# Kernel optimization log

Hardware: AMD Instinct MI355X
Metric: run time of the kernel (lower is better)

## Reference

```python
import jax, jax.numpy as jnp
import numpy as np

def setup_inputs() -> dict:
    key = jax.random.key(0)
    k1, k2, k3 = jax.random.split(key, 3)
    N, C, H, W = 16, 128, 128, 128
    out_chn = 128
    x = jax.random.normal(k1, (N, C, H, W), dtype=jnp.float32)
    # 1x1 conv = per-pixel linear: weight (out_chn, in_chn), bias (out_chn,)
    fan_in = C  # kernel_size=1 -> fan_in = in_chn
    bound = 1.0 / np.sqrt(fan_in)
    conv_w = jax.random.uniform(k2, (out_chn, C), dtype=jnp.float32, minval=-bound, maxval=bound)
    conv_b = jax.random.uniform(k3, (out_chn,), dtype=jnp.float32, minval=-bound, maxval=bound)
    return {"x": x, "conv_w": conv_w, "conv_b": conv_b}

def reference(x, conv_w, conv_b):
    N, C, H, W = x.shape
    x_hw = x.reshape(N, C, H * W)                     # (N, C, HW)
    logits = jnp.einsum('ncl,ndl->ncd', x_hw, x_hw)    # (N, C, C), unscaled
    weights = jax.nn.softmax(logits, axis=-1)
    attn = jnp.einsum('ncd,ndl->ncl', weights, x_hw)   # (N, C, HW)
    attn = attn.reshape(N, C, H, W)
    # 1x1 conv: contract over channel dim
    out = jnp.einsum('nchw,oc->nohw', attn, conv_w) + conv_b[None, :, None, None]
    return out
```

## Files before the change

kernel.cpp:

```cpp
#include <hip/hip_runtime.h>
#include <stdint.h>

#define NB    16
#define CD    128
#define HW    16384
#define KSPLIT 32

typedef float  f32x4  __attribute__((ext_vector_type(4)));
typedef short  bf16x8 __attribute__((ext_vector_type(8)));

__device__ __forceinline__ unsigned f2bf(float f) {
    unsigned u = __float_as_uint(f);
    u += 0x7FFFu + ((u >> 16) & 1u);
    return u >> 16;
}
__device__ __forceinline__ unsigned pk2bf(float a, float b) {
    return f2bf(a) | (f2bf(b) << 16);
}

__global__ __launch_bounds__(256, 2) void gram_kernel(const float* __restrict__ x,
                                                      float* __restrict__ P) {
    const int n  = blockIdx.x;
    const int kc = blockIdx.y;
    const int t    = threadIdx.x;
    const int wv   = t >> 6;
    const int lane = t & 63;
    const int q    = lane >> 4;
    const int r16  = lane & 15;

    __shared__ __align__(16) unsigned short Xl[2 * CD * 128];

    f32x4 acc[4][4];
#pragma unroll
    for (int i = 0; i < 4; ++i)
#pragma unroll
        for (int j = 0; j < 4; ++j) acc[i][j] = (f32x4)0.0f;

    const int rt0 = 4 * (wv >> 1);
    const int ct0 = 4 * (wv & 1);

    const float* xb = x + (size_t)n * CD * HW;

    const int cS  = t >> 5;
    const int lS  = (t & 31) * 4;
    const int wsw = lS ^ (8 * cS);
    const int rx  = 8 * (r16 & 7);

    float4 stg[16];
#pragma unroll
    for (int i = 0; i < 16; ++i)
        stg[i] = *(const float4*)(xb + (size_t)(i * 8 + cS) * HW + kc * 512 + lS);
#pragma unroll
    for (int i = 0; i < 16; ++i) {
        uint2 pk;
        pk.x = pk2bf(stg[i].x, stg[i].y);
        pk.y = pk2bf(stg[i].z, stg[i].w);
        *(uint2*)(&Xl[(i * 8 + cS) * 128 + wsw]) = pk;
    }

    for (int sub = 0; sub < 4; ++sub) {
        if (sub < 3) {
            const int kb = kc * 512 + (sub + 1) * 128;
#pragma unroll
            for (int i = 0; i < 16; ++i)
                stg[i] = *(const float4*)(xb + (size_t)(i * 8 + cS) * HW + kb + lS);
        }
        __syncthreads();

        const unsigned short* Xc = &Xl[(size_t)(sub & 1) * CD * 128];
#pragma unroll
        for (int ks = 0; ks < 4; ++ks) {
            const int ko = (ks * 32 + q * 8) ^ rx;
            bf16x8 af[4], bfr[4];
#pragma unroll
            for (int i = 0; i < 4; ++i) {
                union { bf16x8 v; uint4 u; } ua;
                ua.u = *(const uint4*)&Xc[(16 * (rt0 + i) + r16) * 128 + ko];
                af[i] = ua.v;
                union { bf16x8 v; uint4 u; } ub;
                ub.u = *(const uint4*)&Xc[(16 * (ct0 + i) + r16) * 128 + ko];
                bfr[i] = ub.v;
            }
#pragma unroll
            for (int i = 0; i < 4; ++i)
#pragma unroll
                for (int j = 0; j < 4; ++j)
                    acc[i][j] = __builtin_amdgcn_mfma_f32_16x16x32_bf16(
                        af[i], bfr[j], acc[i][j], 0, 0, 0);
        }

        if (sub < 3) {
            unsigned short* Xn = &Xl[(size_t)((sub + 1) & 1) * CD * 128];
#pragma unroll
            for (int i = 0; i < 16; ++i) {
                uint2 pk;
                pk.x = pk2bf(stg[i].x, stg[i].y);
                pk.y = pk2bf(stg[i].z, stg[i].w);
                *(uint2*)(&Xn[(i * 8 + cS) * 128 + wsw]) = pk;
            }
        }
    }

    float* Pn = P + ((size_t)kc * NB + n) * CD * CD;
#pragma unroll
    for (int i = 0; i < 4; ++i)
#pragma unroll
        for (int j = 0; j < 4; ++j)
#pragma unroll
            for (int rr = 0; rr < 4; ++rr) {
                int row = 16 * (rt0 + i) + q * 4 + rr;
                int col = 16 * (ct0 + j) + r16;
                Pn[row * CD + col] = acc[i][j][rr];
            }
}

__global__ __launch_bounds__(256) void reduce_kernel(const float* __restrict__ P,
                                                     float* __restrict__ E) {
    const int R    = blockIdx.x * 4 + (threadIdx.x >> 6);
    const int lane = threadIdx.x & 63;
    const int n    = R >> 7;
    const int row  = R & 127;

    const float* p = P + (size_t)n * CD * CD + (size_t)row * CD + 2 * lane;
    float s0 = 0.0f, s1 = 0.0f;
#pragma unroll
    for (int kc = 0; kc < KSPLIT; ++kc) {
        const float2 v = *(const float2*)(p + (size_t)kc * NB * CD * CD);
        s0 += v.x; s1 += v.y;
    }
    float m = fmaxf(s0, s1);
#pragma unroll
    for (int off = 32; off > 0; off >>= 1) m = fmaxf(m, __shfl_xor(m, off));
    const float e0 = __expf(s0 - m);
    const float e1 = __expf(s1 - m);
    float e = e0 + e1;
#pragma unroll
    for (int off = 32; off > 0; off >>= 1) e += __shfl_xor(e, off);
    const float inv = 1.0f / e;
    float2 st; st.x = e0 * inv; st.y = e1 * inv;
    *(float2*)(E + (size_t)n * CD * CD + (size_t)row * CD + 2 * lane) = st;
}

__global__ __launch_bounds__(256) void mmat_kernel(const float* __restrict__ E,
                                                   const float* __restrict__ cw,
                                                   unsigned short* __restrict__ Mbf) {
    const int n  = blockIdx.x;
    const int bo = blockIdx.y;
    const int t  = threadIdx.x;
    const int o  = bo * 8 + (t >> 5);
    const int d0 = (t & 31) * 4;

    const float* En  = E + (size_t)n * CD * CD;
    const float* cwo = cw + (size_t)o * CD;

    float a0 = 0, a1 = 0, a2 = 0, a3 = 0;
#pragma unroll 8
    for (int c = 0; c < CD; ++c) {
        const float cv = cwo[c];
        float4 w = *(const float4*)&En[c * CD + d0];
        a0 += cv * w.x; a1 += cv * w.y; a2 += cv * w.z; a3 += cv * w.w;
    }
    uint2 pk;
    pk.x = pk2bf(a0, a1);
    pk.y = pk2bf(a2, a3);
    *(uint2*)&Mbf[((size_t)n * CD + o) * CD + d0] = pk;
}

__global__ __launch_bounds__(256) void out_kernel(const float* __restrict__ x,
                                                  const unsigned short* __restrict__ Mbf,
                                                  const float* __restrict__ bias,
                                                  float* __restrict__ out) {
    const int lb = blockIdx.x;
    const int n  = blockIdx.y;
    const int l0 = lb * 128;
    const int t    = threadIdx.x;
    const int wv   = t >> 6;
    const int lane = t & 63;
    const int q    = lane >> 4;
    const int r16  = lane & 15;

    __shared__ __align__(16) unsigned short Xt[128 * 128];
    __shared__ float bl[CD];

    const int lt0 = 4 * (wv >> 1);
    const int ot0 = 4 * (wv & 1);

    if (t < CD) bl[t] = bias[t];

    const float* xb = x + (size_t)n * CD * HW + l0;
    const int lt = t & 31;
    const int dg = t >> 5;
#pragma unroll
    for (int i = 0; i < 4; ++i) {
        const int d0 = i * 32 + dg * 4;
        const float* bp = xb + (size_t)d0 * HW + 4 * lt;
        float4 v0 = *(const float4*)(bp);
        float4 v1 = *(const float4*)(bp + HW);
        float4 v2 = *(const float4*)(bp + 2 * HW);
        float4 v3 = *(const float4*)(bp + 3 * HW);
        float r0[4] = {v0.x, v0.y, v0.z, v0.w};
        float r1[4] = {v1.x, v1.y, v1.z, v1.w};
        float r2[4] = {v2.x, v2.y, v2.z, v2.w};
        float r3[4] = {v3.x, v3.y, v3.z, v3.w};
        const int dph = d0 ^ (8 * (lt & 7));
#pragma unroll
        for (int j = 0; j < 4; ++j) {
            uint2 pk;
            pk.x = pk2bf(r0[j], r1[j]);
            pk.y = pk2bf(r2[j], r3[j]);
            *(uint2*)&Xt[(4 * lt + j) * 128 + dph] = pk;
        }
    }
    __syncthreads();

    f32x4 acc[4][4];
#pragma unroll
    for (int i = 0; i < 4; ++i)
#pragma unroll
        for (int j = 0; j < 4; ++j) acc[i][j] = (f32x4)0.0f;

    const unsigned short* Mn = Mbf + (size_t)n * CD * CD;
#pragma unroll
    for (int ks = 0; ks < 4; ++ks) {
        const int k0 = ks * 32 + q * 8;
        bf16x8 bfr[4];
#pragma unroll
        for (int j = 0; j < 4; ++j) {
            const int o = 16 * (ot0 + j) + r16;
            union { bf16x8 v; uint4 u; } ub;
            ub.u = *(const uint4*)&Mn[o * CD + k0];
            bfr[j] = ub.v;
        }
        bf16x8 af[4];
#pragma unroll
        for (int i = 0; i < 4; ++i) {
            const int l = 16 * (lt0 + i) + r16;
            const int doff = k0 ^ (8 * ((l >> 2) & 7));
            union { bf16x8 v; uint4 u; } ua;
            ua.u = *(const uint4*)&Xt[l * 128 + doff];
            af[i] = ua.v;
        }
#pragma unroll
        for (int i = 0; i < 4; ++i)
#pragma unroll
            for (int j = 0; j < 4; ++j)
                acc[i][j] = __builtin_amdgcn_mfma_f32_16x16x32_bf16(
                    af[i], bfr[j], acc[i][j], 0, 0, 0);
    }

    float* ob = out + (size_t)n * CD * HW + l0;
#pragma unroll
    for (int i = 0; i < 4; ++i)
#pragma unroll
        for (int j = 0; j < 4; ++j) {
            const int o = 16 * (ot0 + j) + r16;
            const int l = 16 * (lt0 + i) + q * 4;
            const float b = bl[o];
            float4 st;
            st.x = acc[i][j][0] + b;
            st.y = acc[i][j][1] + b;
            st.z = acc[i][j][2] + b;
            st.w = acc[i][j][3] + b;
            *(float4*)(ob + (size_t)o * HW + l) = st;
        }
}

extern "C" void kernel_launch(void* const* d_in, const int* in_sizes, int n_in,
                              void* d_out, int out_size, void* d_ws, size_t ws_size,
                              hipStream_t stream) {
    const float* x  = (const float*)d_in[0];
    const float* cw = (const float*)d_in[1];
    const float* cb = (const float*)d_in[2];
    float* out = (float*)d_out;

    char* ws = (char*)d_ws;
    float*          P   = (float*)(ws);
    float*          E   = (float*)(ws + (32u << 20));
    unsigned short* Mbf = (unsigned short*)(ws + (33u << 20));

    gram_kernel   <<<dim3(NB, KSPLIT), 256, 0, stream>>>(x, P);
    reduce_kernel <<<dim3(512),        256, 0, stream>>>(P, E);
    mmat_kernel   <<<dim3(NB, 16),     256, 0, stream>>>(E, cw, Mbf);
    out_kernel    <<<dim3(128, NB),    256, 0, stream>>>(x, Mbf, cb, out);
}
```

Baseline: 300.8 us.

## Fuse reduce, mmat and output kernels into one persistent ticketed tail kernel

Replaces three separate launches (softmax reduce, mixing-matrix build, output GEMM) with a single kernel whose blocks take atomic tickets and synchronize through global counters, spin-waiting on flags between stages. Flags are reset by the first gram block. This removes two kernel launch boundaries and lets output blocks start staging x as soon as dependencies resolve, at the cost of spin-wait overhead and a reliance on ticket ordering for forward progress.

New measurement: 665.1 us. 2.21x slower.

```diff
diff --git a/kernel.cpp b/kernel.cpp
--- a/kernel.cpp
+++ b/kernel.cpp
@@ -19,7 +19,8 @@
 }
 
 __global__ __launch_bounds__(256, 2) void gram_kernel(const float* __restrict__ x,
-                                                      float* __restrict__ P) {
+                                                      float* __restrict__ P,
+                                                      unsigned* __restrict__ flags) {
     const int n  = blockIdx.x;
     const int kc = blockIdx.y;
     const int t    = threadIdx.x;
@@ -28,13 +29,9 @@
     const int q    = lane >> 4;
     const int r16  = lane & 15;
 
+    if (n == 0 && kc == 0 && t < 3) flags[t * 16] = 0u;
+
     __shared__ __align__(16) unsigned short Xl[2 * CD * 128];
-
-    f32x4 acc[4][4];
-#pragma unroll
-    for (int i = 0; i < 4; ++i)
-#pragma unroll
-        for (int j = 0; j < 4; ++j) acc[i][j] = (f32x4)0.0f;
 
     const int rt0 = 4 * (wv >> 1);
     const int ct0 = 4 * (wv & 1);
@@ -45,6 +42,12 @@
     const int lS  = (t & 31) * 4;
     const int wsw = lS ^ (8 * cS);
     const int rx  = 8 * (r16 & 7);
+
+    f32x4 acc[4][4];
+#pragma unroll
+    for (int i = 0; i < 4; ++i)
+#pragma unroll
+        for (int j = 0; j < 4; ++j) acc[i][j] = (f32x4)0.0f;
 
     float4 stg[16];
 #pragma unroll
@@ -114,155 +117,176 @@
             }
 }
 
-__global__ __launch_bounds__(256) void reduce_kernel(const float* __restrict__ P,
-                                                     float* __restrict__ E) {
-    const int R    = blockIdx.x * 4 + (threadIdx.x >> 6);
-    const int lane = threadIdx.x & 63;
-    const int n    = R >> 7;
-    const int row  = R & 127;
-
-    const float* p = P + (size_t)n * CD * CD + (size_t)row * CD + 2 * lane;
-    float s0 = 0.0f, s1 = 0.0f;
-#pragma unroll
-    for (int kc = 0; kc < KSPLIT; ++kc) {
-        const float2 v = *(const float2*)(p + (size_t)kc * NB * CD * CD);
-        s0 += v.x; s1 += v.y;
-    }
-    float m = fmaxf(s0, s1);
-#pragma unroll
-    for (int off = 32; off > 0; off >>= 1) m = fmaxf(m, __shfl_xor(m, off));
-    const float e0 = __expf(s0 - m);
-    const float e1 = __expf(s1 - m);
-    float e = e0 + e1;
-#pragma unroll
-    for (int off = 32; off > 0; off >>= 1) e += __shfl_xor(e, off);
-    const float inv = 1.0f / e;
-    float2 st; st.x = e0 * inv; st.y = e1 * inv;
-    *(float2*)(E + (size_t)n * CD * CD + (size_t)row * CD + 2 * lane) = st;
-}
-
-__global__ __launch_bounds__(256) void mmat_kernel(const float* __restrict__ E,
-                                                   const float* __restrict__ cw,
-                                                   unsigned short* __restrict__ Mbf) {
-    const int n  = blockIdx.x;
-    const int bo = blockIdx.y;
-    const int t  = threadIdx.x;
-    const int o  = bo * 8 + (t >> 5);
-    const int d0 = (t & 31) * 4;
-
-    const float* En  = E + (size_t)n * CD * CD;
-    const float* cwo = cw + (size_t)o * CD;
-
-    float a0 = 0, a1 = 0, a2 = 0, a3 = 0;
-#pragma unroll 8
-    for (int c = 0; c < CD; ++c) {
-        const float cv = cwo[c];
-        float4 w = *(const float4*)&En[c * CD + d0];
-        a0 += cv * w.x; a1 += cv * w.y; a2 += cv * w.z; a3 += cv * w.w;
-    }
-    uint2 pk;
-    pk.x = pk2bf(a0, a1);
-    pk.y = pk2bf(a2, a3);
-    *(uint2*)&Mbf[((size_t)n * CD + o) * CD + d0] = pk;
-}
-
-__global__ __launch_bounds__(256) void out_kernel(const float* __restrict__ x,
-                                                  const unsigned short* __restrict__ Mbf,
-                                                  const float* __restrict__ bias,
-                                                  float* __restrict__ out) {
-    const int lb = blockIdx.x;
-    const int n  = blockIdx.y;
-    const int l0 = lb * 128;
-    const int t    = threadIdx.x;
-    const int wv   = t >> 6;
-    const int lane = t & 63;
-    const int q    = lane >> 4;
-    const int r16  = lane & 15;
-
+__global__ __launch_bounds__(256, 4) void tail_kernel(
+    const float* __restrict__ P, const float* __restrict__ x,
+    const float* __restrict__ cw, const float* __restrict__ cb,
+    float* __restrict__ E, unsigned short* __restrict__ Mbf,
+    float* __restrict__ out, unsigned* __restrict__ flags)
+{
+    const int t = threadIdx.x;
+    __shared__ unsigned s_tk;
     __shared__ __align__(16) unsigned short Xt[128 * 128];
     __shared__ float bl[CD];
 
-    const int lt0 = 4 * (wv >> 1);
-    const int ot0 = 4 * (wv & 1);
-
-    if (t < CD) bl[t] = bias[t];
-
-    const float* xb = x + (size_t)n * CD * HW + l0;
-    const int lt = t & 31;
-    const int dg = t >> 5;
-#pragma unroll
-    for (int i = 0; i < 4; ++i) {
-        const int d0 = i * 32 + dg * 4;
-        const float* bp = xb + (size_t)d0 * HW + 4 * lt;
-        float4 v0 = *(const float4*)(bp);
-        float4 v1 = *(const float4*)(bp + HW);
-        float4 v2 = *(const float4*)(bp + 2 * HW);
-        float4 v3 = *(const float4*)(bp + 3 * HW);
-        float r0[4] = {v0.x, v0.y, v0.z, v0.w};
-        float r1[4] = {v1.x, v1.y, v1.z, v1.w};
-        float r2[4] = {v2.x, v2.y, v2.z, v2.w};
-        float r3[4] = {v3.x, v3.y, v3.z, v3.w};
-        const int dph = d0 ^ (8 * (lt & 7));
-#pragma unroll
-        for (int j = 0; j < 4; ++j) {
-            uint2 pk;
-            pk.x = pk2bf(r0[j], r1[j]);
-            pk.y = pk2bf(r2[j], r3[j]);
-            *(uint2*)&Xt[(4 * lt + j) * 128 + dph] = pk;
-        }
-    }
+    if (t == 0) s_tk = atomicAdd(&flags[0], 1u);
     __syncthreads();
-
-    f32x4 acc[4][4];
-#pragma unroll
-    for (int i = 0; i < 4; ++i)
-#pragma unroll
-        for (int j = 0; j < 4; ++j) acc[i][j] = (f32x4)0.0f;
-
-    const unsigned short* Mn = Mbf + (size_t)n * CD * CD;
-#pragma unroll
-    for (int ks = 0; ks < 4; ++ks) {
-        const int k0 = ks * 32 + q * 8;
-        bf16x8 bfr[4];
-#pragma unroll
-        for (int j = 0; j < 4; ++j) {
-            const int o = 16 * (ot0 + j) + r16;
-            union { bf16x8 v; uint4 u; } ub;
-            ub.u = *(const uint4*)&Mn[o * CD + k0];
-            bfr[j] = ub.v;
-        }
-        bf16x8 af[4];
+    const unsigned tk = s_tk;
+
+    if (tk < 512u) {
+        const int R    = (int)tk * 4 + (t >> 6);
+        const int lane = t & 63;
+        const int n    = R >> 7;
+        const int row  = R & 127;
+        const float* p = P + (size_t)n * CD * CD + (size_t)row * CD + 2 * lane;
+        float s0 = 0.0f, s1 = 0.0f;
+#pragma unroll
+        for (int kc = 0; kc < KSPLIT; ++kc) {
+            const float2 v = *(const float2*)(p + (size_t)kc * NB * CD * CD);
+            s0 += v.x; s1 += v.y;
+        }
+        float m = fmaxf(s0, s1);
+#pragma unroll
+        for (int off = 32; off > 0; off >>= 1) m = fmaxf(m, __shfl_xor(m, off));
+        const float e0 = __expf(s0 - m);
+        const float e1 = __expf(s1 - m);
+        float e = e0 + e1;
+#pragma unroll
+        for (int off = 32; off > 0; off >>= 1) e += __shfl_xor(e, off);
+        const float inv = 1.0f / e;
+        float2 st; st.x = e0 * inv; st.y = e1 * inv;
+        *(float2*)(E + (size_t)n * CD * CD + (size_t)row * CD + 2 * lane) = st;
+
+        __threadfence();
+        __syncthreads();
+        if (t == 0) atomicAdd(&flags[16], 1u);
+    }
+
+    if (tk >= 512u && tk < 768u) {
+        if (t == 0)
+            while (atomicAdd(&flags[16], 0u) < 512u) __builtin_amdgcn_s_sleep(32);
+        __syncthreads();
+        __threadfence();
+
+        const unsigned u = tk - 512u;
+        const int n  = (int)(u >> 4);
+        const int bo = (int)(u & 15u);
+        const int o  = bo * 8 + (t >> 5);
+        const int d0 = (t & 31) * 4;
+        const float* En  = E + (size_t)n * CD * CD;
+        const float* cwo = cw + (size_t)o * CD;
+        float a0 = 0, a1 = 0, a2 = 0, a3 = 0;
+#pragma unroll 8
+        for (int c = 0; c < CD; ++c) {
+            const float cv = cwo[c];
+            float4 w = *(const float4*)&En[c * CD + d0];
+            a0 += cv * w.x; a1 += cv * w.y; a2 += cv * w.z; a3 += cv * w.w;
+        }
+        uint2 pk;
+        pk.x = pk2bf(a0, a1);
+        pk.y = pk2bf(a2, a3);
+        *(uint2*)&Mbf[((size_t)n * CD + o) * CD + d0] = pk;
+
+        __threadfence();
+        __syncthreads();
+        if (t == 0) atomicAdd(&flags[32], 1u);
+    }
+
+    if (t == 0)
+        while (atomicAdd(&flags[32], 0u) < 256u) __builtin_amdgcn_s_sleep(32);
+    __syncthreads();
+    __threadfence();
+
+    {
+        const int lb = (int)(tk & 127u);
+        const int n  = (int)(tk >> 7);
+        const int l0 = lb * 128;
+        const int wv   = t >> 6;
+        const int lane = t & 63;
+        const int q    = lane >> 4;
+        const int r16  = lane & 15;
+
+        const int lt0 = 4 * (wv >> 1);
+        const int ot0 = 4 * (wv & 1);
+
+        if (t < CD) bl[t] = cb[t];
+
+        const float* xb = x + (size_t)n * CD * HW + l0;
+        const int lt = t & 31;
+        const int dg = t >> 5;
 #pragma unroll
         for (int i = 0; i < 4; ++i) {
-            const int l = 16 * (lt0 + i) + r16;
-            const int doff = k0 ^ (8 * ((l >> 2) & 7));
-            union { bf16x8 v; uint4 u; } ua;
-            ua.u = *(const uint4*)&Xt[l * 128 + doff];
-            af[i] = ua.v;
-        }
+            const int d0 = i * 32 + dg * 4;
+            const float* bp = xb + (size_t)d0 * HW + 4 * lt;
+            float4 v0 = *(const float4*)(bp);
+            float4 v1 = *(const float4*)(bp + HW);
+            float4 v2 = *(const float4*)(bp + 2 * HW);
+            float4 v3 = *(const float4*)(bp + 3 * HW);
+            float r0[4] = {v0.x, v0.y, v0.z, v0.w};
+            float r1[4] = {v1.x, v1.y, v1.z, v1.w};
+            float r2[4] = {v2.x, v2.y, v2.z, v2.w};
+            float r3[4] = {v3.x, v3.y, v3.z, v3.w};
+            const int dph = d0 ^ (8 * (lt & 7));
+#pragma unroll
+            for (int j = 0; j < 4; ++j) {
+                uint2 pk;
+                pk.x = pk2bf(r0[j], r1[j]);
+                pk.y = pk2bf(r2[j], r3[j]);
+                *(uint2*)&Xt[(4 * lt + j) * 128 + dph] = pk;
+            }
+        }
+        __syncthreads();
+
+        f32x4 acc[4][4];
 #pragma unroll
         for (int i = 0; i < 4; ++i)
 #pragma unroll
-            for (int j = 0; j < 4; ++j)
-                acc[i][j] = __builtin_amdgcn_mfma_f32_16x16x32_bf16(
-                    af[i], bfr[j], acc[i][j], 0, 0, 0);
-    }
-
-    float* ob = out + (size_t)n * CD * HW + l0;
-#pragma unroll
-    for (int i = 0; i < 4; ++i)
-#pragma unroll
-        for (int j = 0; j < 4; ++j) {
-            const int o = 16 * (ot0 + j) + r16;
-            const int l = 16 * (lt0 + i) + q * 4;
-            const float b = bl[o];
-            float4 st;
-            st.x = acc[i][j][0] + b;
-            st.y = acc[i][j][1] + b;
-            st.z = acc[i][j][2] + b;
-            st.w = acc[i][j][3] + b;
-            *(float4*)(ob + (size_t)o * HW + l) = st;
-        }
+            for (int j = 0; j < 4; ++j) acc[i][j] = (f32x4)0.0f;
+
+        const unsigned short* Mn = Mbf + (size_t)n * CD * CD;
+#pragma unroll
+        for (int ks = 0; ks < 4; ++ks) {
+            const int k0 = ks * 32 + q * 8;
+            bf16x8 bfr[4];
+#pragma unroll
+            for (int j = 0; j < 4; ++j) {
+                const int o = 16 * (ot0 + j) + r16;
+                union { bf16x8 v; uint4 u; } ub;
+                ub.u = *(const uint4*)&Mn[o * CD + k0];
+                bfr[j] = ub.v;
+            }
+            bf16x8 af[4];
+#pragma unroll
+            for (int i = 0; i < 4; ++i) {
+                const int l = 16 * (lt0 + i) + r16;
+                const int doff = k0 ^ (8 * ((l >> 2) & 7));
+                union { bf16x8 v; uint4 u; } ua;
+                ua.u = *(const uint4*)&Xt[l * 128 + doff];
+                af[i] = ua.v;
+            }
+#pragma unroll
+            for (int i = 0; i < 4; ++i)
+#pragma unroll
+                for (int j = 0; j < 4; ++j)
+                    acc[i][j] = __builtin_amdgcn_mfma_f32_16x16x32_bf16(
+                        af[i], bfr[j], acc[i][j], 0, 0, 0);
+        }
+
+        float* ob = out + (size_t)n * CD * HW + l0;
+#pragma unroll
+        for (int i = 0; i < 4; ++i)
+#pragma unroll
+            for (int j = 0; j < 4; ++j) {
+                const int o = 16 * (ot0 + j) + r16;
+                const int l = 16 * (lt0 + i) + q * 4;
+                const float b = bl[o];
+                float4 st;
+                st.x = acc[i][j][0] + b;
+                st.y = acc[i][j][1] + b;
+                st.z = acc[i][j][2] + b;
+                st.w = acc[i][j][3] + b;
+                *(float4*)(ob + (size_t)o * HW + l) = st;
+            }
+    }
 }
 
 extern "C" void kernel_launch(void* const* d_in, const int* in_sizes, int n_in,
@@ -274,12 +298,12 @@
     float* out = (float*)d_out;
 
     char* ws = (char*)d_ws;
-    float*          P   = (float*)(ws);
-    float*          E   = (float*)(ws + (32u << 20));
-    unsigned short* Mbf = (unsigned short*)(ws + (33u << 20));
-
-    gram_kernel   <<<dim3(NB, KSPLIT), 256, 0, stream>>>(x, P);
-    reduce_kernel <<<dim3(512),        256, 0, stream>>>(P, E);
-    mmat_kernel   <<<dim3(NB, 16),     256, 0, stream>>>(E, cw, Mbf);
-    out_kernel    <<<dim3(128, NB),    256, 0, stream>>>(x, Mbf, cb, out);
-}
+    float*          P     = (float*)(ws);
+    float*          E     = (float*)(ws + (32u << 20));
+    unsigned short* Mbf   = (unsigned short*)(ws + (33u << 20));
+    unsigned*       flags = (unsigned*)(ws + (34u << 20));
+
+    gram_kernel <<<dim3(NB, KSPLIT), 256, 0, stream>>>(x, P, flags);
+    tail_kernel <<<dim3(2048),       256, 0, stream>>>(P, x, cw, cb, E, Mbf,
+                                                       out, flags);
+}
```
